# Optimization experiments

Hardware: AMD Instinct MI355X
Metric: run time of the kernel (lower is better)

## Reference

```python
import jax, jax.numpy as jnp
import numpy as np

B, L, K, M, N, P, D = 8, 512, 512, 64, 64, 64, 64  # M == D required for residual add


def _layernorm(x, gamma, beta, eps=1e-3):  # keras LayerNormalization default eps
    mu = jnp.mean(x, axis=-1, keepdims=True)
    var = jnp.var(x, axis=-1, keepdims=True)
    return (x - mu) * jax.lax.rsqrt(var + eps) * gamma + beta


def setup_inputs() -> dict:
    key = jax.random.key(0)
    ks = jax.random.split(key, 5)
    return {
        "q": jax.random.normal(ks[0], (B, L, D), dtype=jnp.float32),
        "k": jax.random.normal(ks[1], (B, K, D), dtype=jnp.float32),
        "vq": jax.random.normal(ks[2], (B, L, M, N), dtype=jnp.float32),
        "vk": jax.random.normal(ks[3], (B, K, P, N), dtype=jnp.float32),
        "vexp": jax.random.normal(ks[4], (B, K, P), dtype=jnp.float32),
        "scale": jnp.ones((), dtype=jnp.float32),      # keras Attention use_scale param (init 1)
        "ln_gamma": jnp.ones((D,), dtype=jnp.float32),  # LayerNormalization gamma
        "ln_beta": jnp.zeros((D,), dtype=jnp.float32),  # LayerNormalization beta
    }


def reference(q, k, vq, vk, vexp, scale, ln_gamma, ln_beta):
    # scores: keras Attention with use_scale -> scale * q @ k^T  (B, L, K)
    scores = scale * jnp.einsum('bld,bkd->blk', q, k)
    # no mask in this call path; plain softmax over keys
    weights = jax.nn.softmax(scores, axis=-1)

    # Original value path (materializes 5D 'blkmp'):
    #   s1 = einsum('blmn,bkpn->blkmp', vq, vk)
    #   v  = einsum('blkmp,bkp->blkm', s1, vexp)
    #   out = einsum('blk,blkm->blm', weights, v)
    # Mathematically identical reassociation that never builds the 5D tensor:
    vkc = jnp.einsum('bkpn,bkp->bkn', vk, vexp)       # contract P first
    tmp = jnp.einsum('blk,bkn->bln', weights, vkc)    # softmax-weighted combine over K
    attn_out = jnp.einsum('blmn,bln->blm', vq, tmp)   # contract N -> (B, L, M)

    # BaseAttentionCell / CrossAttention: residual add + LayerNorm
    return _layernorm(q + attn_out, ln_gamma, ln_beta)
```

## Files before the change

kernel.cpp:

```cpp
#include <hip/hip_runtime.h>


__global__ __launch_bounds__(256) void vkc_kernel(const float* __restrict__ vk,
                                                  const float* __restrict__ vexp,
                                                  float* __restrict__ vkc) {
    const int wave = (blockIdx.x << 2) + (threadIdx.x >> 6);
    const int lane = threadIdx.x & 63;

    const float ve_reg = vexp[wave * 64 + lane];
    const int n0 = (lane & 15) << 2;
    const float* base = vk + (long)wave * 4096;

    float ax = 0.f, ay = 0.f, az = 0.f, aw = 0.f;
    #pragma unroll
    for (int it = 0; it < 16; ++it) {
        const int p = (lane >> 4) + (it << 2);
        const float4 v4 = *(const float4*)(base + p * 64 + n0);
        const float w = __shfl(ve_reg, p, 64);
        ax += v4.x * w; ay += v4.y * w; az += v4.z * w; aw += v4.w * w;
    }
    ax += __shfl_down(ax, 32, 64); ax += __shfl_down(ax, 16, 64);
    ay += __shfl_down(ay, 32, 64); ay += __shfl_down(ay, 16, 64);
    az += __shfl_down(az, 32, 64); az += __shfl_down(az, 16, 64);
    aw += __shfl_down(aw, 32, 64); aw += __shfl_down(aw, 16, 64);

    if ((lane & 48) == 0) {
        float4 r; r.x = ax; r.y = ay; r.z = az; r.w = aw;
        *(float4*)(vkc + wave * 64 + n0) = r;
    }
}

__global__ __launch_bounds__(512) void score_tmp_kernel(const float* __restrict__ q,
                                                        const float* __restrict__ k,
                                                        const float* __restrict__ vkc,
                                                        const float* __restrict__ scale_p,
                                                        float* __restrict__ tmp_g) {
    __shared__ float sc[8][512];
    __shared__ float tp[8][8][64];

    const int t = threadIdx.x;
    const int wv = t >> 6;
    const int lane = t & 63;
    const int batch = blockIdx.x >> 6;
    const int l0 = (blockIdx.x & 63) << 3;

    const float scale = scale_p[0];
    const float* qbase = q + (batch * 512 + l0) * 64;

    {
        const float4* krow = (const float4*)(k + (batch * 512 + t) * 64);
        float acc[8] = {0.f, 0.f, 0.f, 0.f, 0.f, 0.f, 0.f, 0.f};
        #pragma unroll
        for (int dc = 0; dc < 16; ++dc) {
            const float4 kv = krow[dc];
            #pragma unroll
            for (int l = 0; l < 8; ++l) {
                const float4 qv = ((const float4*)(qbase + l * 64))[dc];
                acc[l] += qv.x * kv.x + qv.y * kv.y + qv.z * kv.z + qv.w * kv.w;
            }
        }
        #pragma unroll
        for (int l = 0; l < 8; ++l) sc[l][t] = scale * acc[l];
    }
    __syncthreads();

    {
        float v[8]; float mx = -1e30f;
        #pragma unroll
        for (int j = 0; j < 8; ++j) { v[j] = sc[wv][lane + 64 * j]; mx = fmaxf(mx, v[j]); }
        #pragma unroll
        for (int off = 32; off; off >>= 1) mx = fmaxf(mx, __shfl_xor(mx, off, 64));
        float s = 0.f;
        #pragma unroll
        for (int j = 0; j < 8; ++j) { v[j] = __expf(v[j] - mx); s += v[j]; }
        #pragma unroll
        for (int off = 32; off; off >>= 1) s += __shfl_xor(s, off, 64);
        const float inv = 1.0f / s;
        #pragma unroll
        for (int j = 0; j < 8; ++j) sc[wv][lane + 64 * j] = v[j] * inv;
    }
    __syncthreads();

    {
        const float* vkcb = vkc + batch * 512 * 64;
        const int ksub = lane >> 4;
        const int n0 = (lane & 15) << 2;
        const int kbeg = wv << 6;
        float4 a[8];
        #pragma unroll
        for (int l = 0; l < 8; ++l) { a[l].x = 0.f; a[l].y = 0.f; a[l].z = 0.f; a[l].w = 0.f; }
        #pragma unroll
        for (int i = 0; i < 16; ++i) {
            const int kk = kbeg + (i << 2) + ksub;
            const float4 v4 = *(const float4*)(vkcb + kk * 64 + n0);
            #pragma unroll
            for (int l = 0; l < 8; ++l) {
                const float w = sc[l][kk];
                a[l].x += w * v4.x; a[l].y += w * v4.y;
                a[l].z += w * v4.z; a[l].w += w * v4.w;
            }
        }
        #pragma unroll
        for (int l = 0; l < 8; ++l) {
            a[l].x += __shfl_down(a[l].x, 32, 64); a[l].x += __shfl_down(a[l].x, 16, 64);
            a[l].y += __shfl_down(a[l].y, 32, 64); a[l].y += __shfl_down(a[l].y, 16, 64);
            a[l].z += __shfl_down(a[l].z, 32, 64); a[l].z += __shfl_down(a[l].z, 16, 64);
            a[l].w += __shfl_down(a[l].w, 32, 64); a[l].w += __shfl_down(a[l].w, 16, 64);
        }
        if (lane < 16) {
            #pragma unroll
            for (int l = 0; l < 8; ++l)
                *(float4*)&tp[wv][l][lane << 2] = a[l];
        }
    }
    __syncthreads();
    {
        float s = tp[0][wv][lane];
        #pragma unroll
        for (int w = 1; w < 8; ++w) s += tp[w][wv][lane];
        tmp_g[(batch * 512 + l0) * 64 + t] = s;
    }
}

__global__ __launch_bounds__(256) void out_kernel(const float* __restrict__ q,
                                                  const float* __restrict__ vq,
                                                  const float* __restrict__ tmp_g,
                                                  const float* __restrict__ gamma,
                                                  const float* __restrict__ beta,
                                                  float* __restrict__ out) {
    __shared__ float attn_s[4][64];

    const int wv = threadIdx.x >> 6;
    const int lane = threadIdx.x & 63;
    const int row = (blockIdx.x << 2) + wv;

    const float* vql = vq + (long)row * 4096;

    float4 v[16];
    #pragma unroll
    for (int it = 0; it < 16; ++it)
        v[it] = *(const float4*)(vql + it * 256 + lane * 4);

    const float qv = q[row * 64 + lane];
    const int n0 = (lane & 15) << 2;
    const float4 t4 = *(const float4*)(tmp_g + row * 64 + n0);

    #pragma unroll
    for (int it = 0; it < 16; ++it) {
        float part = v[it].x * t4.x + v[it].y * t4.y + v[it].z * t4.z + v[it].w * t4.w;
        part += __shfl_down(part, 8, 16);
        part += __shfl_down(part, 4, 16);
        part += __shfl_down(part, 2, 16);
        part += __shfl_down(part, 1, 16);
        if ((lane & 15) == 0) attn_s[wv][it * 4 + (lane >> 4)] = part;
    }

    const float x = qv + attn_s[wv][lane];
    float s1 = x, s2 = x * x;
    #pragma unroll
    for (int off = 32; off; off >>= 1) {
        s1 += __shfl_xor(s1, off, 64);
        s2 += __shfl_xor(s2, off, 64);
    }
    const float mean = s1 * (1.0f / 64.0f);
    const float var = s2 * (1.0f / 64.0f) - mean * mean;
    const float r = rsqrtf(var + 1e-3f);
    out[row * 64 + lane] = (x - mean) * r * gamma[lane] + beta[lane];
}

extern "C" void kernel_launch(void* const* d_in, const int* in_sizes, int n_in,
                              void* d_out, int out_size, void* d_ws, size_t ws_size,
                              hipStream_t stream) {
    const float* q     = (const float*)d_in[0];
    const float* k     = (const float*)d_in[1];
    const float* vq    = (const float*)d_in[2];
    const float* vk    = (const float*)d_in[3];
    const float* vexp  = (const float*)d_in[4];
    const float* scale = (const float*)d_in[5];
    const float* gamma = (const float*)d_in[6];
    const float* beta  = (const float*)d_in[7];
    float* out = (float*)d_out;

    float* vkc = (float*)d_ws;
    float* tmp = vkc + 8 * 512 * 64;

    vkc_kernel<<<1024, 256, 0, stream>>>(vk, vexp, vkc);
    score_tmp_kernel<<<512, 512, 0, stream>>>(q, k, vkc, scale, tmp);
    out_kernel<<<1024, 256, 0, stream>>>(q, vq, tmp, gamma, beta, out);
}
```

Before: 180.0 us.

## Compute scores and softmax alongside vkc reduction, stage weights through global memory

```diff
diff --git a/kernel.cpp b/kernel.cpp
--- a/kernel.cpp
+++ b/kernel.cpp
@@ -1,40 +1,105 @@
 #include <hip/hip_runtime.h>
 
 
-__global__ __launch_bounds__(256) void vkc_kernel(const float* __restrict__ vk,
+__global__ __launch_bounds__(512) void pre_kernel(const float* __restrict__ q,
+                                                  const float* __restrict__ k,
+                                                  const float* __restrict__ vk,
                                                   const float* __restrict__ vexp,
-                                                  float* __restrict__ vkc) {
-    const int wave = (blockIdx.x << 2) + (threadIdx.x >> 6);
-    const int lane = threadIdx.x & 63;
-
-    const float ve_reg = vexp[wave * 64 + lane];
-    const int n0 = (lane & 15) << 2;
-    const float* base = vk + (long)wave * 4096;
-
-    float ax = 0.f, ay = 0.f, az = 0.f, aw = 0.f;
-    #pragma unroll
-    for (int it = 0; it < 16; ++it) {
-        const int p = (lane >> 4) + (it << 2);
-        const float4 v4 = *(const float4*)(base + p * 64 + n0);
-        const float w = __shfl(ve_reg, p, 64);
-        ax += v4.x * w; ay += v4.y * w; az += v4.z * w; aw += v4.w * w;
-    }
-    ax += __shfl_down(ax, 32, 64); ax += __shfl_down(ax, 16, 64);
-    ay += __shfl_down(ay, 32, 64); ay += __shfl_down(ay, 16, 64);
-    az += __shfl_down(az, 32, 64); az += __shfl_down(az, 16, 64);
-    aw += __shfl_down(aw, 32, 64); aw += __shfl_down(aw, 16, 64);
-
-    if ((lane & 48) == 0) {
-        float4 r; r.x = ax; r.y = ay; r.z = az; r.w = aw;
-        *(float4*)(vkc + wave * 64 + n0) = r;
-    }
-}
-
-__global__ __launch_bounds__(512) void score_tmp_kernel(const float* __restrict__ q,
-                                                        const float* __restrict__ k,
-                                                        const float* __restrict__ vkc,
-                                                        const float* __restrict__ scale_p,
-                                                        float* __restrict__ tmp_g) {
+                                                  const float* __restrict__ scale_p,
+                                                  float* __restrict__ vkc,
+                                                  float* __restrict__ wts) {
+    const int t = threadIdx.x;
+    const int wv = t >> 6;
+    const int lane = t & 63;
+    const int blk = blockIdx.x;
+
+    if (wv < 4) {
+        #pragma unroll
+        for (int r = 0; r < 2; ++r) {
+            const int row = (blk << 3) + (wv << 1) + r;
+            const float ve = vexp[row * 64 + lane];
+            const int n0 = (lane & 15) << 2;
+            const float* base = vk + (long)row * 4096;
+            float ax = 0.f, ay = 0.f, az = 0.f, aw = 0.f;
+            #pragma unroll
+            for (int it = 0; it < 16; ++it) {
+                const int p = (lane >> 4) + (it << 2);
+                const float4 v4 = *(const float4*)(base + p * 64 + n0);
+                const float w = __shfl(ve, p, 64);
+                ax += v4.x * w; ay += v4.y * w; az += v4.z * w; aw += v4.w * w;
+            }
+            ax += __shfl_down(ax, 32, 64); ax += __shfl_down(ax, 16, 64);
+            ay += __shfl_down(ay, 32, 64); ay += __shfl_down(ay, 16, 64);
+            az += __shfl_down(az, 32, 64); az += __shfl_down(az, 16, 64);
+            aw += __shfl_down(aw, 32, 64); aw += __shfl_down(aw, 16, 64);
+            if ((lane & 48) == 0) {
+                float4 rr; rr.x = ax; rr.y = ay; rr.z = az; rr.w = aw;
+                *(float4*)(vkc + row * 64 + n0) = rr;
+            }
+        }
+    } else {
+        const int batch = blk >> 6;
+        const int l0 = (blk & 63) << 3;
+        const int lw = l0 + ((wv - 4) << 1);
+        const float scale = scale_p[0];
+        const float* kb = k + batch * 512 * 64;
+        const float* q0 = q + (batch * 512 + lw) * 64;
+        const float* q1 = q0 + 64;
+
+        float a0[8], a1[8];
+        #pragma unroll
+        for (int c = 0; c < 8; ++c) {
+            const float4* krow = (const float4*)(kb + ((c << 6) + lane) * 64);
+            float s0 = 0.f, s1 = 0.f;
+            #pragma unroll
+            for (int dc = 0; dc < 16; ++dc) {
+                const float4 kv = krow[dc];
+                const float4 qa = ((const float4*)q0)[dc];
+                const float4 qb = ((const float4*)q1)[dc];
+                s0 += qa.x * kv.x + qa.y * kv.y + qa.z * kv.z + qa.w * kv.w;
+                s1 += qb.x * kv.x + qb.y * kv.y + qb.z * kv.z + qb.w * kv.w;
+            }
+            a0[c] = scale * s0;
+            a1[c] = scale * s1;
+        }
+        {
+            float mx = -1e30f;
+            #pragma unroll
+            for (int c = 0; c < 8; ++c) mx = fmaxf(mx, a0[c]);
+            #pragma unroll
+            for (int off = 32; off; off >>= 1) mx = fmaxf(mx, __shfl_xor(mx, off, 64));
+            float s = 0.f;
+            #pragma unroll
+            for (int c = 0; c < 8; ++c) { a0[c] = __expf(a0[c] - mx); s += a0[c]; }
+            #pragma unroll
+            for (int off = 32; off; off >>= 1) s += __shfl_xor(s, off, 64);
+            const float inv = 1.0f / s;
+            float* wrow = wts + (long)(batch * 512 + lw) * 512;
+            #pragma unroll
+            for (int c = 0; c < 8; ++c) wrow[(c << 6) + lane] = a0[c] * inv;
+        }
+        {
+            float mx = -1e30f;
+            #pragma unroll
+            for (int c = 0; c < 8; ++c) mx = fmaxf(mx, a1[c]);
+            #pragma unroll
+            for (int off = 32; off; off >>= 1) mx = fmaxf(mx, __shfl_xor(mx, off, 64));
+            float s = 0.f;
+            #pragma unroll
+            for (int c = 0; c < 8; ++c) { a1[c] = __expf(a1[c] - mx); s += a1[c]; }
+            #pragma unroll
+            for (int off = 32; off; off >>= 1) s += __shfl_xor(s, off, 64);
+            const float inv = 1.0f / s;
+            float* wrow = wts + (long)(batch * 512 + lw + 1) * 512;
+            #pragma unroll
+            for (int c = 0; c < 8; ++c) wrow[(c << 6) + lane] = a1[c] * inv;
+        }
+    }
+}
+
+__global__ __launch_bounds__(512) void tmp_kernel(const float* __restrict__ vkc,
+                                                  const float* __restrict__ wts,
+                                                  float* __restrict__ tmp_g) {
     __shared__ float sc[8][512];
     __shared__ float tp[8][8][64];
 
@@ -44,40 +109,11 @@
     const int batch = blockIdx.x >> 6;
     const int l0 = (blockIdx.x & 63) << 3;
 
-    const float scale = scale_p[0];
-    const float* qbase = q + (batch * 512 + l0) * 64;
-
     {
-        const float4* krow = (const float4*)(k + (batch * 512 + t) * 64);
-        float acc[8] = {0.f, 0.f, 0.f, 0.f, 0.f, 0.f, 0.f, 0.f};
-        #pragma unroll
-        for (int dc = 0; dc < 16; ++dc) {
-            const float4 kv = krow[dc];
-            #pragma unroll
-            for (int l = 0; l < 8; ++l) {
-                const float4 qv = ((const float4*)(qbase + l * 64))[dc];
-                acc[l] += qv.x * kv.x + qv.y * kv.y + qv.z * kv.z + qv.w * kv.w;
-            }
-        }
-        #pragma unroll
-        for (int l = 0; l < 8; ++l) sc[l][t] = scale * acc[l];
-    }
-    __syncthreads();
-
-    {
-        float v[8]; float mx = -1e30f;
-        #pragma unroll
-        for (int j = 0; j < 8; ++j) { v[j] = sc[wv][lane + 64 * j]; mx = fmaxf(mx, v[j]); }
-        #pragma unroll
-        for (int off = 32; off; off >>= 1) mx = fmaxf(mx, __shfl_xor(mx, off, 64));
-        float s = 0.f;
-        #pragma unroll
-        for (int j = 0; j < 8; ++j) { v[j] = __expf(v[j] - mx); s += v[j]; }
-        #pragma unroll
-        for (int off = 32; off; off >>= 1) s += __shfl_xor(s, off, 64);
-        const float inv = 1.0f / s;
-        #pragma unroll
-        for (int j = 0; j < 8; ++j) sc[wv][lane + 64 * j] = v[j] * inv;
+        const float4* wg = (const float4*)(wts + (long)(batch * 512 + l0) * 512);
+        float4* scf = (float4*)sc;
+        scf[t] = wg[t];
+        scf[t + 512] = wg[t + 512];
     }
     __syncthreads();
 
@@ -182,9 +218,10 @@
     float* out = (float*)d_out;
 
     float* vkc = (float*)d_ws;
-    float* tmp = vkc + 8 * 512 * 64;
-
-    vkc_kernel<<<1024, 256, 0, stream>>>(vk, vexp, vkc);
-    score_tmp_kernel<<<512, 512, 0, stream>>>(q, k, vkc, scale, tmp);
+    float* wts = vkc + 8 * 512 * 64;
+    float* tmp = wts + 8 * 512 * 512;
+
+    pre_kernel<<<512, 512, 0, stream>>>(q, k, vk, vexp, scale, vkc, wts);
+    tmp_kernel<<<512, 512, 0, stream>>>(vkc, wts, tmp);
     out_kernel<<<1024, 256, 0, stream>>>(q, vq, tmp, gamma, beta, out);
 }
```

Result: slower. 201.6 us (+12.0%).
